# Optimization experiments

Hardware: AMD Instinct MI355X
Metric: run time of the kernel (lower is better)

## Reference

```python
import jax, jax.numpy as jnp
import numpy as np

IN_DIM = 256
K = 64
NB = 64  # num_blocks
N = NB * K
BATCH = 4096
DT = 0.05
TAU_EPS = 1e-6


def setup_inputs() -> dict:
    key = jax.random.key(0)
    ks = jax.random.split(key, 10)
    def xavier(k_, shape, fan_in, fan_out):
        lim = np.sqrt(6.0 / (fan_in + fan_out))
        return jax.random.uniform(k_, shape, jnp.float32, -lim, lim)
    return {
        "y": jax.random.normal(ks[0], (BATCH, N), jnp.float32),
        "u_t": jax.random.normal(ks[1], (BATCH, IN_DIM), jnp.float32),
        "tau_raw": jnp.zeros((N,), jnp.float32),
        "W_in_w": xavier(ks[2], (K, IN_DIM), IN_DIM, K),
        "W_in_b": jnp.zeros((K,), jnp.float32),
        "W_fwd_w": xavier(ks[3], (NB - 1, K, K), K, K),
        "W_fwd_b": jnp.zeros((NB - 1, K), jnp.float32),
        "W_rec_w": xavier(ks[4], (NB, K, K), K, K),
        "W_rec_b": jnp.zeros((NB, K), jnp.float32),
        "E_l": xavier(ks[5], (NB, K, K), K, K),
        "E_l_r": xavier(ks[6], (NB, K, K), K, K),
    }


def reference(y, u_t, tau_raw, W_in_w, W_in_b, W_fwd_w, W_fwd_b, W_rec_w, W_rec_b, E_l, E_l_r):
    yb = y.reshape(-1, NB, K)  # [batch, B, k]
    tau = jax.nn.softplus(tau_raw).reshape(NB, K) + TAU_EPS  # [B, k]
    # input drive for block 0 (torch Linear: x @ W^T + b)
    net0 = jnp.tanh(u_t @ W_in_w.T + W_in_b)  # [batch, k]
    # forward coupling for blocks 1..B-1, batched over blocks
    prev = yb[:, :-1, :]  # [batch, B-1, k]
    net_fwd = jnp.tanh(jnp.einsum('bji,joi->bjo', prev, W_fwd_w) + W_fwd_b)
    net_out = jnp.concatenate([net0[:, None, :], net_fwd], axis=1)  # [batch, B, k]
    # recurrent coupling, all blocks
    net_rec = jnp.tanh(jnp.einsum('bji,joi->bjo', yb, W_rec_w) + W_rec_b)
    decay = 1.0 / tau + jnp.abs(net_out) + jnp.abs(net_rec)  # [batch, B, k]
    drive = jnp.einsum('joi,bji->bjo', E_l, net_out) + jnp.einsum('joi,bji->bjo', E_l_r, net_rec)
    y_new = (yb + DT * drive) / (1.0 + DT * decay)
    return y_new.reshape(-1, N)
```

## Files before the change

### kernel.cpp

```cpp
#include <hip/hip_runtime.h>


#define IN_DIM 256
#define K 64
#define NB 64
#define BATCH 4096
#define NTOT (NB * K)
#define DTC 0.05f
#define TAU_EPS 1e-6f
#define LDSTR 72

typedef __bf16 bf16;
typedef bf16 bf16x8 __attribute__((ext_vector_type(8)));
typedef bf16 bf16x4 __attribute__((ext_vector_type(4)));
typedef float f32x4 __attribute__((ext_vector_type(4)));

__device__ __forceinline__ float fast_tanh(float x) {
    float e = __expf(2.0f * x);
    return 1.0f - 2.0f * __builtin_amdgcn_rcpf(e + 1.0f);
}

__device__ __forceinline__ void stage64(bf16* __restrict__ dst,
                                        const float* __restrict__ src,
                                        int gstride, int tid) {
#pragma unroll
    for (int it = 0; it < 4; ++it) {
        int idx = it * 256 + tid;
        int r = idx >> 4;
        int c4 = idx & 15;
        float4 v = *(const float4*)(src + r * gstride + (c4 << 2));
        bf16x4 p = { (bf16)v.x, (bf16)v.y, (bf16)v.z, (bf16)v.w };
        *(bf16x4*)(dst + r * LDSTR + (c4 << 2)) = p;
    }
}

__global__ __launch_bounds__(256)
void ltcn_kernel(const float* __restrict__ y, const float* __restrict__ u_t,
                 const float* __restrict__ tau_raw,
                 const float* __restrict__ W_in_w, const float* __restrict__ W_in_b,
                 const float* __restrict__ W_fwd_w, const float* __restrict__ W_fwd_b,
                 const float* __restrict__ W_rec_w, const float* __restrict__ W_rec_b,
                 const float* __restrict__ E_l, const float* __restrict__ E_l_r,
                 float* __restrict__ out) {
    __shared__ bf16 sY  [64 * LDSTR];
    __shared__ bf16 sP  [64 * LDSTR];
    __shared__ bf16 sWf [64 * LDSTR];
    __shared__ bf16 sWr [64 * LDSTR];
    __shared__ bf16 sEl [64 * LDSTR];
    __shared__ bf16 sElr[64 * LDSTR];
    __shared__ float sInvTau[64], sBf[64], sBr[64];

    const int tid  = threadIdx.x;
    const int j    = blockIdx.y;
    const int b0   = blockIdx.x * 64;
    const int wave = tid >> 6;
    const int lane = tid & 63;
    const int quad = lane >> 4;
    const int l16  = lane & 15;

    stage64(sY,   y       + (size_t)b0 * NTOT + j * K, NTOT, tid);
    stage64(sWr,  W_rec_w + (size_t)j * K * K,          K,   tid);
    stage64(sEl,  E_l     + (size_t)j * K * K,          K,   tid);
    stage64(sElr, E_l_r   + (size_t)j * K * K,          K,   tid);
    if (tid < 64) {
        float x = tau_raw[j * K + tid];
        float sp = (x > 15.0f) ? x : log1pf(__expf(x));
        sInvTau[tid] = 1.0f / (sp + TAU_EPS);
        sBf[tid] = (j == 0) ? W_in_b[tid] : W_fwd_b[(j - 1) * K + tid];
        sBr[tid] = W_rec_b[j * K + tid];
    }

    const int aoff = (wave * 16 + l16) * LDSTR + quad * 8;

    f32x4 accF[4] = {};
    const int rounds = (j == 0) ? 4 : 1;
    for (int kc = 0; kc < rounds; ++kc) {
        if (j == 0) {
            stage64(sP,  u_t    + (size_t)b0 * IN_DIM + kc * 64, IN_DIM, tid);
            stage64(sWf, W_in_w + kc * 64,                        IN_DIM, tid);
        } else {
            stage64(sP,  y       + (size_t)b0 * NTOT + (j - 1) * K, NTOT, tid);
            stage64(sWf, W_fwd_w + (size_t)(j - 1) * K * K,          K,   tid);
        }
        __syncthreads();
#pragma unroll
        for (int k0 = 0; k0 < 64; k0 += 32) {
            bf16x8 a = *(const bf16x8*)(sP + aoff + k0);
#pragma unroll
            for (int ct = 0; ct < 4; ++ct) {
                bf16x8 b = *(const bf16x8*)(sWf + (ct * 16 + l16) * LDSTR + quad * 8 + k0);
                accF[ct] = __builtin_amdgcn_mfma_f32_16x16x32_bf16(a, b, accF[ct], 0, 0, 0);
            }
        }
        __syncthreads();
    }

    f32x4 accR[4] = {};
#pragma unroll
    for (int k0 = 0; k0 < 64; k0 += 32) {
        bf16x8 a = *(const bf16x8*)(sY + aoff + k0);
#pragma unroll
        for (int ct = 0; ct < 4; ++ct) {
            bf16x8 b = *(const bf16x8*)(sWr + (ct * 16 + l16) * LDSTR + quad * 8 + k0);
            accR[ct] = __builtin_amdgcn_mfma_f32_16x16x32_bf16(a, b, accR[ct], 0, 0, 0);
        }
    }

#pragma unroll
    for (int ct = 0; ct < 4; ++ct) {
#pragma unroll
        for (int r = 0; r < 4; ++r) {
            int m = wave * 16 + quad * 4 + r;
            int n = ct * 16 + l16;
            float no = fast_tanh(accF[ct][r] + sBf[n]);
            float nr = fast_tanh(accR[ct][r] + sBr[n]);
            sWf[m * LDSTR + n] = (bf16)no;
            sP [m * LDSTR + n] = (bf16)nr;
        }
    }
    __syncthreads();

    f32x4 accD[4] = {};
#pragma unroll
    for (int k0 = 0; k0 < 64; k0 += 32) {
        bf16x8 aO = *(const bf16x8*)(sWf + aoff + k0);
        bf16x8 aR = *(const bf16x8*)(sP  + aoff + k0);
#pragma unroll
        for (int ct = 0; ct < 4; ++ct) {
            bf16x8 bO = *(const bf16x8*)(sEl  + (ct * 16 + l16) * LDSTR + quad * 8 + k0);
            accD[ct] = __builtin_amdgcn_mfma_f32_16x16x32_bf16(aO, bO, accD[ct], 0, 0, 0);
            bf16x8 bR = *(const bf16x8*)(sElr + (ct * 16 + l16) * LDSTR + quad * 8 + k0);
            accD[ct] = __builtin_amdgcn_mfma_f32_16x16x32_bf16(aR, bR, accD[ct], 0, 0, 0);
        }
    }

#pragma unroll
    for (int ct = 0; ct < 4; ++ct) {
#pragma unroll
        for (int r = 0; r < 4; ++r) {
            int m = wave * 16 + quad * 4 + r;
            int n = ct * 16 + l16;
            size_t gi = (size_t)(b0 + m) * NTOT + j * K + n;
            float yv = y[gi];
            float no = (float)sWf[m * LDSTR + n];
            float nr = (float)sP [m * LDSTR + n];
            float decay = sInvTau[n] + fabsf(no) + fabsf(nr);
            float drive = accD[ct][r];
            out[gi] = (yv + DTC * drive) * __builtin_amdgcn_rcpf(1.0f + DTC * decay);
        }
    }
}

extern "C" void kernel_launch(void* const* d_in, const int* in_sizes, int n_in,
                              void* d_out, int out_size, void* d_ws, size_t ws_size,
                              hipStream_t stream) {
    const float* y       = (const float*)d_in[0];
    const float* u_t     = (const float*)d_in[1];
    const float* tau_raw = (const float*)d_in[2];
    const float* W_in_w  = (const float*)d_in[3];
    const float* W_in_b  = (const float*)d_in[4];
    const float* W_fwd_w = (const float*)d_in[5];
    const float* W_fwd_b = (const float*)d_in[6];
    const float* W_rec_w = (const float*)d_in[7];
    const float* W_rec_b = (const float*)d_in[8];
    const float* E_l     = (const float*)d_in[9];
    const float* E_l_r   = (const float*)d_in[10];
    float* out = (float*)d_out;

    dim3 grid(BATCH / 64, NB);
    hipLaunchKernelGGL(ltcn_kernel, grid, dim3(256), 0, stream,
                       y, u_t, tau_raw, W_in_w, W_in_b, W_fwd_w, W_fwd_b,
                       W_rec_w, W_rec_b, E_l, E_l_r, out);
}
```

Baseline: 180.1 us.

## Load MFMA A-fragments directly from global, drop activation LDS staging

The y and u_t activation tiles are now loaded straight from global memory into per-lane bf16 MFMA A-fragments in registers instead of being staged through shared memory. This removes two LDS buffers and several barriers, and reuses sWr as scratch for the tanh outputs. The decay term is kept in fp32 registers rather than being read back from bf16 LDS, and y for the epilogue is prefetched early. The kernel also gets an occupancy hint of 4 blocks per CU, at the cost of more register pressure and less coalesced fragment loads.

```diff
diff --git a/kernel.cpp b/kernel.cpp
--- a/kernel.cpp
+++ b/kernel.cpp
@@ -34,7 +34,19 @@
     }
 }
 
-__global__ __launch_bounds__(256)
+__device__ __forceinline__ void load_afrag(const float* __restrict__ rowp,
+                                           bf16x8& f0, bf16x8& f1) {
+    float4 a0 = *(const float4*)(rowp);
+    float4 a1 = *(const float4*)(rowp + 4);
+    float4 a2 = *(const float4*)(rowp + 32);
+    float4 a3 = *(const float4*)(rowp + 36);
+    f0 = (bf16x8){ (bf16)a0.x, (bf16)a0.y, (bf16)a0.z, (bf16)a0.w,
+                   (bf16)a1.x, (bf16)a1.y, (bf16)a1.z, (bf16)a1.w };
+    f1 = (bf16x8){ (bf16)a2.x, (bf16)a2.y, (bf16)a2.z, (bf16)a2.w,
+                   (bf16)a3.x, (bf16)a3.y, (bf16)a3.z, (bf16)a3.w };
+}
+
+__global__ __launch_bounds__(256, 4)
 void ltcn_kernel(const float* __restrict__ y, const float* __restrict__ u_t,
                  const float* __restrict__ tau_raw,
                  const float* __restrict__ W_in_w, const float* __restrict__ W_in_b,
@@ -42,8 +54,6 @@
                  const float* __restrict__ W_rec_w, const float* __restrict__ W_rec_b,
                  const float* __restrict__ E_l, const float* __restrict__ E_l_r,
                  float* __restrict__ out) {
-    __shared__ bf16 sY  [64 * LDSTR];
-    __shared__ bf16 sP  [64 * LDSTR];
     __shared__ bf16 sWf [64 * LDSTR];
     __shared__ bf16 sWr [64 * LDSTR];
     __shared__ bf16 sEl [64 * LDSTR];
@@ -57,11 +67,23 @@
     const int lane = tid & 63;
     const int quad = lane >> 4;
     const int l16  = lane & 15;
-
-    stage64(sY,   y       + (size_t)b0 * NTOT + j * K, NTOT, tid);
-    stage64(sWr,  W_rec_w + (size_t)j * K * K,          K,   tid);
-    stage64(sEl,  E_l     + (size_t)j * K * K,          K,   tid);
-    stage64(sElr, E_l_r   + (size_t)j * K * K,          K,   tid);
+    const int am   = wave * 16 + l16;
+
+    stage64(sWr,  W_rec_w + (size_t)j * K * K, K, tid);
+    stage64(sEl,  E_l     + (size_t)j * K * K, K, tid);
+    stage64(sElr, E_l_r   + (size_t)j * K * K, K, tid);
+
+    bf16x8 yc0, yc1;
+    load_afrag(y + (size_t)(b0 + am) * NTOT + j * K + quad * 8, yc0, yc1);
+
+    bf16x8 yp0, yp1;
+    if (j != 0) {
+        stage64(sWf, W_fwd_w + (size_t)(j - 1) * K * K, K, tid);
+        load_afrag(y + (size_t)(b0 + am) * NTOT + (j - 1) * K + quad * 8, yp0, yp1);
+    } else {
+        stage64(sWf, W_in_w, IN_DIM, tid);
+        load_afrag(u_t + (size_t)(b0 + am) * IN_DIM + quad * 8, yp0, yp1);
+    }
     if (tid < 64) {
         float x = tau_raw[j * K + tid];
         float sp = (x > 15.0f) ? x : log1pf(__expf(x));
@@ -69,42 +91,58 @@
         sBf[tid] = (j == 0) ? W_in_b[tid] : W_fwd_b[(j - 1) * K + tid];
         sBr[tid] = W_rec_b[j * K + tid];
     }
-
-    const int aoff = (wave * 16 + l16) * LDSTR + quad * 8;
-
-    f32x4 accF[4] = {};
-    const int rounds = (j == 0) ? 4 : 1;
-    for (int kc = 0; kc < rounds; ++kc) {
-        if (j == 0) {
-            stage64(sP,  u_t    + (size_t)b0 * IN_DIM + kc * 64, IN_DIM, tid);
-            stage64(sWf, W_in_w + kc * 64,                        IN_DIM, tid);
-        } else {
-            stage64(sP,  y       + (size_t)b0 * NTOT + (j - 1) * K, NTOT, tid);
-            stage64(sWf, W_fwd_w + (size_t)(j - 1) * K * K,          K,   tid);
-        }
-        __syncthreads();
-#pragma unroll
-        for (int k0 = 0; k0 < 64; k0 += 32) {
-            bf16x8 a = *(const bf16x8*)(sP + aoff + k0);
+    __syncthreads();
+
+    f32x4 accF[4] = {}, accR[4] = {};
+    const int boff = quad * 8;
+    if (j != 0) {
+#pragma unroll
+        for (int ct = 0; ct < 4; ++ct) {
+            const bf16* br = sWr + (ct * 16 + l16) * LDSTR + boff;
+            const bf16* bw = sWf + (ct * 16 + l16) * LDSTR + boff;
+            accR[ct] = __builtin_amdgcn_mfma_f32_16x16x32_bf16(yc0, *(const bf16x8*)br,        accR[ct], 0, 0, 0);
+            accR[ct] = __builtin_amdgcn_mfma_f32_16x16x32_bf16(yc1, *(const bf16x8*)(br + 32), accR[ct], 0, 0, 0);
+            accF[ct] = __builtin_amdgcn_mfma_f32_16x16x32_bf16(yp0, *(const bf16x8*)bw,        accF[ct], 0, 0, 0);
+            accF[ct] = __builtin_amdgcn_mfma_f32_16x16x32_bf16(yp1, *(const bf16x8*)(bw + 32), accF[ct], 0, 0, 0);
+        }
+    } else {
+#pragma unroll
+        for (int ct = 0; ct < 4; ++ct) {
+            const bf16* br = sWr + (ct * 16 + l16) * LDSTR + boff;
+            accR[ct] = __builtin_amdgcn_mfma_f32_16x16x32_bf16(yc0, *(const bf16x8*)br,        accR[ct], 0, 0, 0);
+            accR[ct] = __builtin_amdgcn_mfma_f32_16x16x32_bf16(yc1, *(const bf16x8*)(br + 32), accR[ct], 0, 0, 0);
+        }
+        for (int kc = 0; kc < 4; ++kc) {
 #pragma unroll
             for (int ct = 0; ct < 4; ++ct) {
-                bf16x8 b = *(const bf16x8*)(sWf + (ct * 16 + l16) * LDSTR + quad * 8 + k0);
-                accF[ct] = __builtin_amdgcn_mfma_f32_16x16x32_bf16(a, b, accF[ct], 0, 0, 0);
+                const bf16* bw = sWf + (ct * 16 + l16) * LDSTR + boff;
+                accF[ct] = __builtin_amdgcn_mfma_f32_16x16x32_bf16(yp0, *(const bf16x8*)bw,        accF[ct], 0, 0, 0);
+                accF[ct] = __builtin_amdgcn_mfma_f32_16x16x32_bf16(yp1, *(const bf16x8*)(bw + 32), accF[ct], 0, 0, 0);
             }
-        }
-        __syncthreads();
-    }
-
-    f32x4 accR[4] = {};
-#pragma unroll
-    for (int k0 = 0; k0 < 64; k0 += 32) {
-        bf16x8 a = *(const bf16x8*)(sY + aoff + k0);
-#pragma unroll
-        for (int ct = 0; ct < 4; ++ct) {
-            bf16x8 b = *(const bf16x8*)(sWr + (ct * 16 + l16) * LDSTR + quad * 8 + k0);
-            accR[ct] = __builtin_amdgcn_mfma_f32_16x16x32_bf16(a, b, accR[ct], 0, 0, 0);
-        }
-    }
+            if (kc < 3) {
+                load_afrag(u_t + (size_t)(b0 + am) * IN_DIM + (kc + 1) * 64 + quad * 8, yp0, yp1);
+                __syncthreads();
+                stage64(sWf, W_in_w + (kc + 1) * 64, IN_DIM, tid);
+                __syncthreads();
+            }
+        }
+    }
+
+    float absum[4][4];
+#pragma unroll
+    for (int ct = 0; ct < 4; ++ct) {
+        float bfv = sBf[ct * 16 + l16];
+        float brv = sBr[ct * 16 + l16];
+#pragma unroll
+        for (int r = 0; r < 4; ++r) {
+            float no = fast_tanh(accF[ct][r] + bfv);
+            float nr = fast_tanh(accR[ct][r] + brv);
+            accF[ct][r] = no;
+            accR[ct][r] = nr;
+            absum[ct][r] = fabsf(no) + fabsf(nr);
+        }
+    }
+    __syncthreads();
 
 #pragma unroll
     for (int ct = 0; ct < 4; ++ct) {
@@ -112,41 +150,47 @@
         for (int r = 0; r < 4; ++r) {
             int m = wave * 16 + quad * 4 + r;
             int n = ct * 16 + l16;
-            float no = fast_tanh(accF[ct][r] + sBf[n]);
-            float nr = fast_tanh(accR[ct][r] + sBr[n]);
-            sWf[m * LDSTR + n] = (bf16)no;
-            sP [m * LDSTR + n] = (bf16)nr;
+            sWf[m * LDSTR + n] = (bf16)accF[ct][r];
+            sWr[m * LDSTR + n] = (bf16)accR[ct][r];
         }
     }
     __syncthreads();
 
+    float ye[4][4];
+    const float* yep = y + (size_t)(b0 + wave * 16 + quad * 4) * NTOT + (size_t)j * K + l16;
+#pragma unroll
+    for (int ct = 0; ct < 4; ++ct)
+#pragma unroll
+        for (int r = 0; r < 4; ++r)
+            ye[ct][r] = yep[(size_t)r * NTOT + ct * 16];
+
+    const bf16* aOp = sWf + am * LDSTR + quad * 8;
+    const bf16* aRp = sWr + am * LDSTR + quad * 8;
+    bf16x8 aO0 = *(const bf16x8*)aOp,        aO1 = *(const bf16x8*)(aOp + 32);
+    bf16x8 aR0 = *(const bf16x8*)aRp,        aR1 = *(const bf16x8*)(aRp + 32);
+
     f32x4 accD[4] = {};
 #pragma unroll
-    for (int k0 = 0; k0 < 64; k0 += 32) {
-        bf16x8 aO = *(const bf16x8*)(sWf + aoff + k0);
-        bf16x8 aR = *(const bf16x8*)(sP  + aoff + k0);
-#pragma unroll
-        for (int ct = 0; ct < 4; ++ct) {
-            bf16x8 bO = *(const bf16x8*)(sEl  + (ct * 16 + l16) * LDSTR + quad * 8 + k0);
-            accD[ct] = __builtin_amdgcn_mfma_f32_16x16x32_bf16(aO, bO, accD[ct], 0, 0, 0);
-            bf16x8 bR = *(const bf16x8*)(sElr + (ct * 16 + l16) * LDSTR + quad * 8 + k0);
-            accD[ct] = __builtin_amdgcn_mfma_f32_16x16x32_bf16(aR, bR, accD[ct], 0, 0, 0);
-        }
-    }
+    for (int ct = 0; ct < 4; ++ct) {
+        const bf16* bo = sEl  + (ct * 16 + l16) * LDSTR + quad * 8;
+        const bf16* br = sElr + (ct * 16 + l16) * LDSTR + quad * 8;
+        accD[ct] = __builtin_amdgcn_mfma_f32_16x16x32_bf16(aO0, *(const bf16x8*)bo,        accD[ct], 0, 0, 0);
+        accD[ct] = __builtin_amdgcn_mfma_f32_16x16x32_bf16(aO1, *(const bf16x8*)(bo + 32), accD[ct], 0, 0, 0);
+        accD[ct] = __builtin_amdgcn_mfma_f32_16x16x32_bf16(aR0, *(const bf16x8*)br,        accD[ct], 0, 0, 0);
+        accD[ct] = __builtin_amdgcn_mfma_f32_16x16x32_bf16(aR1, *(const bf16x8*)(br + 32), accD[ct], 0, 0, 0);
+    }
+
+    float it4[4];
+#pragma unroll
+    for (int ct = 0; ct < 4; ++ct) it4[ct] = sInvTau[ct * 16 + l16];
 
 #pragma unroll
     for (int ct = 0; ct < 4; ++ct) {
 #pragma unroll
         for (int r = 0; r < 4; ++r) {
-            int m = wave * 16 + quad * 4 + r;
-            int n = ct * 16 + l16;
-            size_t gi = (size_t)(b0 + m) * NTOT + j * K + n;
-            float yv = y[gi];
-            float no = (float)sWf[m * LDSTR + n];
-            float nr = (float)sP [m * LDSTR + n];
-            float decay = sInvTau[n] + fabsf(no) + fabsf(nr);
-            float drive = accD[ct][r];
-            out[gi] = (yv + DTC * drive) * __builtin_amdgcn_rcpf(1.0f + DTC * decay);
+            size_t gi = (size_t)(b0 + wave * 16 + quad * 4 + r) * NTOT + j * K + ct * 16 + l16;
+            float decay = it4[ct] + absum[ct][r];
+            out[gi] = (ye[ct][r] + DTC * accD[ct][r]) * __builtin_amdgcn_rcpf(1.0f + DTC * decay);
         }
     }
 }
```

After: 163.4 us. 1.1x faster.
